# Kernel tuning notes

Hardware: AMD Instinct MI355X
Metric: run time of the kernel (lower is better)

Reference implementation:

```python
import jax, jax.numpy as jnp
import numpy as np

N_HEAD = 16
ROPE_BASE = 10000.0


def _rotate_half(x):
    # interleaved rotate: (-x2, x1) pairs, matching torch stack+flatten
    x1 = x[..., ::2]
    x2 = x[..., 1::2]
    return jnp.stack((-x2, x1), axis=-1).reshape(x.shape)


def setup_inputs() -> dict:
    key = jax.random.key(0)
    ks = jax.random.split(key, 5)
    B, S, C = 4, 2048, 1024
    sc = 1.0 / np.sqrt(C)
    return {
        "x": jax.random.normal(ks[0], (B, S, C), jnp.float32),
        "W_qkv": jax.random.normal(ks[1], (C, 3 * C), jnp.float32) * sc,
        "b_qkv": jax.random.normal(ks[2], (3 * C,), jnp.float32) * 0.02,
        "W_proj": jax.random.normal(ks[3], (C, C), jnp.float32) * sc,
        "b_proj": jax.random.normal(ks[4], (C,), jnp.float32) * 0.02,
    }


def reference(x, W_qkv, b_qkv, W_proj, b_proj):
    B, S, C = x.shape
    H = N_HEAD
    D = C // H

    qkv = x @ W_qkv + b_qkv                       # [B,S,3C]
    q, k, v = jnp.split(qkv, 3, axis=-1)
    q = q.reshape(B, S, H, D).transpose(0, 2, 1, 3)  # [B,H,S,D]
    k = k.reshape(B, S, H, D).transpose(0, 2, 1, 3)
    v = v.reshape(B, S, H, D).transpose(0, 2, 1, 3)

    # RoPE cache (offset=0), faithful to source: emb = cat(freqs, freqs)
    inv_freq = 1.0 / (ROPE_BASE ** (jnp.arange(0, D, 2, dtype=jnp.float32) / D))
    pos = jnp.arange(S, dtype=jnp.float32)
    freqs = jnp.outer(pos, inv_freq)              # [S, D/2]
    emb = jnp.concatenate((freqs, freqs), axis=-1)  # [S, D]
    cos = jnp.cos(emb)[None, None, :, :]
    sin = jnp.sin(emb)[None, None, :, :]

    q = q * cos + _rotate_half(q) * sin
    k = k * cos + _rotate_half(k) * sin

    scale = 1.0 / jnp.sqrt(jnp.asarray(D, x.dtype))
    scores = jnp.einsum("bhqd,bhkd->bhqk", q, k) * scale  # [B,H,S,S]
    causal = jnp.tril(jnp.ones((S, S), dtype=bool))
    scores = jnp.where(causal[None, None], scores, jnp.asarray(-jnp.inf, x.dtype))
    att = jax.nn.softmax(scores, axis=-1)
    out = jnp.einsum("bhqk,bhkd->bhqd", att, v)    # [B,H,S,D]

    out = out.transpose(0, 2, 1, 3).reshape(B, S, C)
    out = out @ W_proj + b_proj                    # dropout=0 (eval)
    return out
```

## Files before the change

kernel.cpp:

```cpp
#include <hip/hip_runtime.h>
#include <hip/hip_bf16.h>
#include <math.h>

#define B_ 4
#define S_ 2048
#define C_ 1024
#define H_ 16
#define D_ 64
#define M_ (B_*S_)
#define NQKV (3*C_)
#define KDIM C_

typedef float f32x4 __attribute__((ext_vector_type(4)));
typedef short bf16x8 __attribute__((ext_vector_type(8)));

static __device__ __forceinline__ ushort f2bf(float f){
    __hip_bfloat16 h = __float2bfloat16(f);
    union { __hip_bfloat16 b; ushort u; } v; v.b = h;
    return v.u;
}

static __device__ __forceinline__ void gload16(const ushort* g, ushort* l){
    __builtin_amdgcn_global_load_lds((__attribute__((address_space(1))) void*)g,
                                     (__attribute__((address_space(3))) void*)l,
                                     16, 0, 0);
}

__global__ void k_conv(const float* __restrict__ in, ushort* __restrict__ out, int n4){
    int i = blockIdx.x*blockDim.x + threadIdx.x;
    if (i < n4){
        float4 v = *(const float4*)(in + i*4);
        ushort4 o;
        o.x = f2bf(v.x); o.y = f2bf(v.y); o.z = f2bf(v.z); o.w = f2bf(v.w);
        *(ushort4*)(out + i*4) = o;
    }
}

__global__ void k_transpose(const float* __restrict__ in, ushort* __restrict__ out,
                            int R, int Ccol){
    __shared__ float tile[32][33];
    int c0 = blockIdx.x*32, r0 = blockIdx.y*32;
    int tx = threadIdx.x, ty = threadIdx.y;
    for (int j = ty; j < 32; j += 8)
        tile[j][tx] = in[(r0 + j)*Ccol + c0 + tx];
    __syncthreads();
    for (int j = ty; j < 32; j += 8)
        out[(size_t)(c0 + tx)*R + r0 + j] = f2bf(tile[j][tx]);
}

__global__ void k_rope_tab(float* __restrict__ cosT, float* __restrict__ sinT){
    int t = blockIdx.x*blockDim.x + threadIdx.x;
    if (t >= S_*D_) return;
    int pos = t >> 6, j = t & 63;
    float invf = powf(10000.0f, -(float)(j & 31) / 32.0f);
    float ang = (float)pos * invf;
    cosT[t] = cosf(ang);
    sinT[t] = sinf(ang);
}


__launch_bounds__(512, 4)
__global__ void k_qkv(const ushort* __restrict__ xb, const ushort* __restrict__ wt,
                      const float* __restrict__ bqkv,
                      const float* __restrict__ cosT, const float* __restrict__ sinT,
                      ushort* __restrict__ qb, ushort* __restrict__ kb, ushort* __restrict__ vT){
    __shared__ __align__(16) ushort As[2][256][32];
    __shared__ __align__(16) ushort Bs[2][128][32];
    int bid = blockIdx.x;
    int lin = (bid & 7)*96 + (bid >> 3);
    int bx = lin % 24, by = lin / 24;
    int M0 = by*256, N0 = bx*128;
    int tid = threadIdx.x;
    int wid = tid >> 6, lane = tid & 63;
    int wm = wid >> 1, wn = wid & 1;
    int lrow = lane & 15, lk = lane >> 4;
    int swu = (lrow >> 1) & 3;

    int scol = (((lane & 3) ^ ((lane >> 3) & 3))) * 8;
    const ushort* gA0 = &xb[(size_t)(M0 + wid*16 + (lane >> 2))*KDIM + scol];
    const ushort* gA1 = gA0 + (size_t)128*KDIM;
    const ushort* gB0 = &wt[(size_t)(N0 + wid*16 + (lane >> 2))*KDIM + scol];

    f32x4 acc[4][4] = {};
    int cur = 0;
    gload16(gA0, &As[0][wid*16][0]);
    gload16(gA1, &As[0][128 + wid*16][0]);
    gload16(gB0, &Bs[0][wid*16][0]);
    __syncthreads();

    for (int k0 = 0; k0 < KDIM; k0 += 32){
        int nk = k0 + 32;
        if (nk < KDIM){
            gload16(gA0 + nk, &As[cur^1][wid*16][0]);
            gload16(gA1 + nk, &As[cur^1][128 + wid*16][0]);
            gload16(gB0 + nk, &Bs[cur^1][wid*16][0]);
        }
        bf16x8 a[4], b[4];
#pragma unroll
        for (int mi = 0; mi < 4; mi++)
            a[mi] = *(const bf16x8*)(&As[cur][wm*64 + mi*16 + lrow][(lk ^ swu)*8]);
#pragma unroll
        for (int ni = 0; ni < 4; ni++)
            b[ni] = *(const bf16x8*)(&Bs[cur][wn*64 + ni*16 + lrow][(lk ^ swu)*8]);
#pragma unroll
        for (int mi = 0; mi < 4; mi++)
#pragma unroll
            for (int ni = 0; ni < 4; ni++)
                acc[mi][ni] = __builtin_amdgcn_mfma_f32_16x16x32_bf16(a[mi], b[ni], acc[mi][ni], 0, 0, 0);
        __syncthreads();
        cur ^= 1;
    }
#pragma unroll
    for (int mi = 0; mi < 4; mi++)
#pragma unroll
    for (int ni = 0; ni < 4; ni++){
        int gn = N0 + wn*64 + ni*16 + lrow;
        float bias = bqkv[gn];
        int which = gn >> 10;
        int cn = gn & 1023;
        int h = cn >> 6, d = cn & 63;
        int gm0 = M0 + wm*64 + mi*16 + lk*4;
        if (which == 2){
            int bb = gm0 >> 11, pos0 = gm0 & 2047;
            ushort4 o = { f2bf(acc[mi][ni][0] + bias), f2bf(acc[mi][ni][1] + bias),
                          f2bf(acc[mi][ni][2] + bias), f2bf(acc[mi][ni][3] + bias) };
            *(ushort4*)(&vT[(((size_t)(bb*H_ + h))*D_ + d)*S_ + pos0]) = o;
        } else {
#pragma unroll
            for (int rr = 0; rr < 4; rr++){
                int gm = gm0 + rr;
                float val = acc[mi][ni][rr] + bias;
                float rot = __shfl_xor(val, 1);
                int bb = gm >> 11, pos = gm & 2047;
                int out_idx = ((((bb*H_ + h)*S_) + pos))*D_ + d;
                float c = cosT[pos*64 + d], s = sinT[pos*64 + d];
                float o = val*c + ((d & 1) ? rot : -rot)*s;
                if (which == 0) o *= 0.18033688f;
                ((which == 0) ? qb : kb)[out_idx] = f2bf(o);
            }
        }
    }
}

__launch_bounds__(512, 4)
__global__ void k_proj(const ushort* __restrict__ ab, const ushort* __restrict__ wt,
                       const float* __restrict__ bias, float* __restrict__ out){
    __shared__ __align__(16) ushort As[2][256][32];
    __shared__ __align__(16) ushort Bs[2][128][32];
    int bid = blockIdx.x;
    int lin = (bid & 7)*32 + (bid >> 3);
    int bx = lin & 7, by = lin >> 3;
    int M0 = by*256, N0 = bx*128;
    int tid = threadIdx.x;
    int wid = tid >> 6, lane = tid & 63;
    int wm = wid >> 1, wn = wid & 1;
    int lrow = lane & 15, lk = lane >> 4;
    int swu = (lrow >> 1) & 3;

    int scol = (((lane & 3) ^ ((lane >> 3) & 3))) * 8;
    const ushort* gA0 = &ab[(size_t)(M0 + wid*16 + (lane >> 2))*KDIM + scol];
    const ushort* gA1 = gA0 + (size_t)128*KDIM;
    const ushort* gB0 = &wt[(size_t)(N0 + wid*16 + (lane >> 2))*KDIM + scol];

    f32x4 acc[4][4] = {};
    int cur = 0;
    gload16(gA0, &As[0][wid*16][0]);
    gload16(gA1, &As[0][128 + wid*16][0]);
    gload16(gB0, &Bs[0][wid*16][0]);
    __syncthreads();

    for (int k0 = 0; k0 < KDIM; k0 += 32){
        int nk = k0 + 32;
        if (nk < KDIM){
            gload16(gA0 + nk, &As[cur^1][wid*16][0]);
            gload16(gA1 + nk, &As[cur^1][128 + wid*16][0]);
            gload16(gB0 + nk, &Bs[cur^1][wid*16][0]);
        }
        bf16x8 a[4], b[4];
#pragma unroll
        for (int mi = 0; mi < 4; mi++)
            a[mi] = *(const bf16x8*)(&As[cur][wm*64 + mi*16 + lrow][(lk ^ swu)*8]);
#pragma unroll
        for (int ni = 0; ni < 4; ni++)
            b[ni] = *(const bf16x8*)(&Bs[cur][wn*64 + ni*16 + lrow][(lk ^ swu)*8]);
#pragma unroll
        for (int mi = 0; mi < 4; mi++)
#pragma unroll
            for (int ni = 0; ni < 4; ni++)
                acc[mi][ni] = __builtin_amdgcn_mfma_f32_16x16x32_bf16(a[mi], b[ni], acc[mi][ni], 0, 0, 0);
        __syncthreads();
        cur ^= 1;
    }
#pragma unroll
    for (int mi = 0; mi < 4; mi++)
#pragma unroll
    for (int ni = 0; ni < 4; ni++){
        int gn = N0 + wn*64 + ni*16 + lrow;
        float bv = bias[gn];
#pragma unroll
        for (int rr = 0; rr < 4; rr++){
            int gm = M0 + wm*64 + mi*16 + lk*4 + rr;
            out[(size_t)gm*C_ + gn] = acc[mi][ni][rr] + bv;
        }
    }
}

__launch_bounds__(256)
__global__ void k_attn(const ushort* __restrict__ qb, const ushort* __restrict__ kb,
                       const ushort* __restrict__ vT, ushort* __restrict__ ob){
    __shared__ __align__(16) ushort Ks[64][64];
    __shared__ __align__(16) ushort Vs[64][64];
    __shared__ __align__(16) ushort ptile[4][16][64];
    int bh = blockIdx.x;
    int qt = (gridDim.y - 1) - blockIdx.y;
    int bb = bh >> 4, h = bh & 15;
    int tid = threadIdx.x, wid = tid >> 6, lane = tid & 63;
    int lrow = lane & 15, lk = lane >> 4;
    int sw = lrow & 7;
    const ushort* qp = qb + (size_t)bh*S_*D_;
    const ushort* kp = kb + (size_t)bh*S_*D_;
    const ushort* vp = vT + (size_t)bh*D_*S_;
    int qrow = qt*64 + wid*16 + lrow;

    bf16x8 fq[2];
    fq[0] = *(const bf16x8*)(&qp[qrow*D_ + lk*8]);
    fq[1] = *(const bf16x8*)(&qp[qrow*D_ + 32 + lk*8]);

    f32x4 acc[4] = {};
    float m = -1e30f, l = 0.0f;

    int tr  = tid >> 3;
    int tcu = tid & 7;
    int twu = (tcu ^ (tr & 7)) * 8;
    int tc  = tcu * 8;

    int4 ra = *(const int4*)(&kp[tr*D_ + tc]);
    int4 rb = *(const int4*)(&kp[(tr + 32)*D_ + tc]);
    int4 rc = *(const int4*)(&vp[(size_t)tr*S_ + tc]);
    int4 rd = *(const int4*)(&vp[(size_t)(tr + 32)*S_ + tc]);

    const int jend = qt*64;
    for (int j0 = 0; ; j0 += 64){
        *(int4*)(&Ks[tr][twu])      = ra;
        *(int4*)(&Ks[tr + 32][twu]) = rb;
        *(int4*)(&Vs[tr][twu])      = rc;
        *(int4*)(&Vs[tr + 32][twu]) = rd;
        __syncthreads();
        bool diag = (j0 == jend);
        if (!diag){
            int j1 = j0 + 64;
            ra = *(const int4*)(&kp[(j1 + tr)*D_ + tc]);
            rb = *(const int4*)(&kp[(j1 + tr + 32)*D_ + tc]);
            rc = *(const int4*)(&vp[(size_t)tr*S_ + j1 + tc]);
            rd = *(const int4*)(&vp[(size_t)(tr + 32)*S_ + j1 + tc]);
        }

        float p[4][4];
        float tmax = -1e30f;
        if (!diag){
#pragma unroll
            for (int s2 = 0; s2 < 4; s2++){
                bf16x8 k0 = *(const bf16x8*)(&Ks[s2*16 + lrow][(lk ^ sw)*8]);
                bf16x8 k1 = *(const bf16x8*)(&Ks[s2*16 + lrow][((4 + lk) ^ sw)*8]);
                f32x4 z = {};
                z = __builtin_amdgcn_mfma_f32_16x16x32_bf16(k0, fq[0], z, 0, 0, 0);
                z = __builtin_amdgcn_mfma_f32_16x16x32_bf16(k1, fq[1], z, 0, 0, 0);
#pragma unroll
                for (int r = 0; r < 4; r++){ p[s2][r] = z[r]; tmax = fmaxf(tmax, z[r]); }
            }
        } else {
#pragma unroll
            for (int s2 = 0; s2 < 4; s2++){
                if (s2 <= wid){
                    bf16x8 k0 = *(const bf16x8*)(&Ks[s2*16 + lrow][(lk ^ sw)*8]);
                    bf16x8 k1 = *(const bf16x8*)(&Ks[s2*16 + lrow][((4 + lk) ^ sw)*8]);
                    f32x4 z = {};
                    z = __builtin_amdgcn_mfma_f32_16x16x32_bf16(k0, fq[0], z, 0, 0, 0);
                    z = __builtin_amdgcn_mfma_f32_16x16x32_bf16(k1, fq[1], z, 0, 0, 0);
#pragma unroll
                    for (int r = 0; r < 4; r++){
                        float v = z[r];
                        if (s2 == wid && (lk*4 + r) > lrow) v = -1e30f;
                        p[s2][r] = v; tmax = fmaxf(tmax, v);
                    }
                } else {
#pragma unroll
                    for (int r = 0; r < 4; r++) p[s2][r] = -1e30f;
                }
            }
        }
        tmax = fmaxf(tmax, __shfl_xor(tmax, 16));
        tmax = fmaxf(tmax, __shfl_xor(tmax, 32));
        if (__any(tmax > m)){
            float newm = fmaxf(m, tmax);
            float resc = exp2f(m - newm);
            m = newm;
            l *= resc;
#pragma unroll
            for (int nt = 0; nt < 4; nt++)
#pragma unroll
                for (int r = 0; r < 4; r++) acc[nt][r] *= resc;
        }
        float rsum = 0.0f;
#pragma unroll
        for (int s2 = 0; s2 < 4; s2++)
#pragma unroll
            for (int r = 0; r < 4; r++){
                float e = exp2f(p[s2][r] - m);
                p[s2][r] = e;
                rsum += e;
            }
        rsum += __shfl_xor(rsum, 16);
        rsum += __shfl_xor(rsum, 32);
        l += rsum;

#pragma unroll
        for (int s2 = 0; s2 < 4; s2++){
            uint2 w;
            w.x = (unsigned)f2bf(p[s2][0]) | ((unsigned)f2bf(p[s2][1]) << 16);
            w.y = (unsigned)f2bf(p[s2][2]) | ((unsigned)f2bf(p[s2][3]) << 16);
            *(uint2*)(&ptile[wid][lrow][((s2*2 + (lk >> 1)) ^ sw)*8 + (lk & 1)*4]) = w;
        }
        bool hi = !diag || (wid >= 2);
        bf16x8 fp0 = *(const bf16x8*)(&ptile[wid][lrow][(lk ^ sw)*8]);
#pragma unroll
        for (int nt = 0; nt < 4; nt++){
            bf16x8 fv0 = *(const bf16x8*)(&Vs[nt*16 + lrow][(lk ^ sw)*8]);
            acc[nt] = __builtin_amdgcn_mfma_f32_16x16x32_bf16(fv0, fp0, acc[nt], 0, 0, 0);
        }
        if (hi){
            bf16x8 fp1 = *(const bf16x8*)(&ptile[wid][lrow][((4 + lk) ^ sw)*8]);
#pragma unroll
            for (int nt = 0; nt < 4; nt++){
                bf16x8 fv1 = *(const bf16x8*)(&Vs[nt*16 + lrow][((4 + lk) ^ sw)*8]);
                acc[nt] = __builtin_amdgcn_mfma_f32_16x16x32_bf16(fv1, fp1, acc[nt], 0, 0, 0);
            }
        }
        __syncthreads();
        if (diag) break;
    }
    float rl = 1.0f / l;
#pragma unroll
    for (int nt = 0; nt < 4; nt++){
        ushort4 o = { f2bf(acc[nt][0]*rl), f2bf(acc[nt][1]*rl),
                      f2bf(acc[nt][2]*rl), f2bf(acc[nt][3]*rl) };
        *(ushort4*)(&ob[((size_t)(bb*S_ + qrow))*C_ + h*D_ + nt*16 + lk*4]) = o;
    }
}

extern "C" void kernel_launch(void* const* d_in, const int* in_sizes, int n_in,
                              void* d_out, int out_size, void* d_ws, size_t ws_size,
                              hipStream_t stream) {
    const float* x     = (const float*)d_in[0];
    const float* Wqkv  = (const float*)d_in[1];
    const float* bqkv  = (const float*)d_in[2];
    const float* Wproj = (const float*)d_in[3];
    const float* bproj = (const float*)d_in[4];
    float* out = (float*)d_out;

    char* ws = (char*)d_ws;
    ushort* xb   = (ushort*)(ws);
    ushort* wqt  = (ushort*)(ws + (16u<<20));
    ushort* wpt  = (ushort*)(ws + (22u<<20));
    float*  cosT = (float*) (ws + (24u<<20));
    float*  sinT = (float*) (ws + (24u<<20) + (512u<<10));
    ushort* qbuf = (ushort*)(ws + (25u<<20));
    ushort* kbuf = (ushort*)(ws + (41u<<20));
    ushort* vbuf = (ushort*)(ws + (57u<<20));
    ushort* obuf = (ushort*)(ws + (73u<<20));

    k_conv<<<(M_*KDIM/4 + 255)/256, 256, 0, stream>>>(x, xb, M_*KDIM/4);
    dim3 tb(32, 8);
    k_transpose<<<dim3(NQKV/32, KDIM/32), tb, 0, stream>>>(Wqkv, wqt, KDIM, NQKV);
    k_transpose<<<dim3(C_/32, KDIM/32), tb, 0, stream>>>(Wproj, wpt, KDIM, C_);
    k_rope_tab<<<(S_*D_ + 255)/256, 256, 0, stream>>>(cosT, sinT);

    k_qkv<<<768, 512, 0, stream>>>(xb, wqt, bqkv, cosT, sinT, qbuf, kbuf, vbuf);
    k_attn<<<dim3(B_*H_, S_/64), 256, 0, stream>>>(qbuf, kbuf, vbuf, obuf);
    k_proj<<<256, 512, 0, stream>>>(obuf, wpt, bproj, out);
}
```

Baseline: 201.3 us.

## Rewrite attention with 32x32 MFMA, 128-row query tiles, register-resident P

The attention kernel now processes 128 query rows per block, with each wave owning 32 rows, and uses 32x32x16 bf16 MFMAs instead of 16x16x32. The softmax probabilities are packed with v_cvt_pk_bf16_f32 and rearranged across lanes with permlane32_swap, so they feed the PV MFMA directly and the LDS P tile round-trip is gone. Each K/V tile loaded into shared memory is now reused by twice as many query rows, cutting global and LDS traffic per query. The costs are higher register pressure, a 3-blocks-per-SM launch bound, half as many blocks (worse load balance on the causal triangle), and waves idling on key tiles past their diagonal.

```diff
diff --git a/kernel.cpp b/kernel.cpp
--- a/kernel.cpp
+++ b/kernel.cpp
@@ -12,6 +12,7 @@
 #define KDIM C_
 
 typedef float f32x4 __attribute__((ext_vector_type(4)));
+typedef float f32x16 __attribute__((ext_vector_type(16)));
 typedef short bf16x8 __attribute__((ext_vector_type(8)));
 
 static __device__ __forceinline__ ushort f2bf(float f){
@@ -57,7 +58,6 @@
     cosT[t] = cosf(ang);
     sinT[t] = sinf(ang);
 }
-
 
 __launch_bounds__(512, 4)
 __global__ void k_qkv(const ushort* __restrict__ xb, const ushort* __restrict__ wt,
@@ -205,146 +205,143 @@
     }
 }
 
-__launch_bounds__(256)
+__launch_bounds__(256, 3)
 __global__ void k_attn(const ushort* __restrict__ qb, const ushort* __restrict__ kb,
                        const ushort* __restrict__ vT, ushort* __restrict__ ob){
     __shared__ __align__(16) ushort Ks[64][64];
     __shared__ __align__(16) ushort Vs[64][64];
-    __shared__ __align__(16) ushort ptile[4][16][64];
     int bh = blockIdx.x;
     int qt = (gridDim.y - 1) - blockIdx.y;
     int bb = bh >> 4, h = bh & 15;
     int tid = threadIdx.x, wid = tid >> 6, lane = tid & 63;
-    int lrow = lane & 15, lk = lane >> 4;
-    int sw = lrow & 7;
+    int lq = lane & 31, hi = lane >> 5;
     const ushort* qp = qb + (size_t)bh*S_*D_;
     const ushort* kp = kb + (size_t)bh*S_*D_;
     const ushort* vp = vT + (size_t)bh*D_*S_;
-    int qrow = qt*64 + wid*16 + lrow;
-
-    bf16x8 fq[2];
-    fq[0] = *(const bf16x8*)(&qp[qrow*D_ + lk*8]);
-    fq[1] = *(const bf16x8*)(&qp[qrow*D_ + 32 + lk*8]);
-
-    f32x4 acc[4] = {};
+    int qw = qt*128 + wid*32;
+    int qrow = qw + lq;
+    int swz = lq & 7;
+
+    bf16x8 fq[4];
+#pragma unroll
+    for (int c = 0; c < 4; c++)
+        fq[c] = *(const bf16x8*)(&qp[qrow*D_ + c*16 + hi*8]);
+
+    f32x16 acc0 = {}, acc1 = {};
     float m = -1e30f, l = 0.0f;
 
-    int tr  = tid >> 3;
-    int tcu = tid & 7;
+    int tr = tid >> 3, tcu = tid & 7;
     int twu = (tcu ^ (tr & 7)) * 8;
-    int tc  = tcu * 8;
+    int tc = tcu * 8;
 
     int4 ra = *(const int4*)(&kp[tr*D_ + tc]);
-    int4 rb = *(const int4*)(&kp[(tr + 32)*D_ + tc]);
+    int4 rb = *(const int4*)(&kp[(tr+32)*D_ + tc]);
     int4 rc = *(const int4*)(&vp[(size_t)tr*S_ + tc]);
-    int4 rd = *(const int4*)(&vp[(size_t)(tr + 32)*S_ + tc]);
-
-    const int jend = qt*64;
-    for (int j0 = 0; ; j0 += 64){
-        *(int4*)(&Ks[tr][twu])      = ra;
-        *(int4*)(&Ks[tr + 32][twu]) = rb;
-        *(int4*)(&Vs[tr][twu])      = rc;
-        *(int4*)(&Vs[tr + 32][twu]) = rd;
+    int4 rd = *(const int4*)(&vp[(size_t)(tr+32)*S_ + tc]);
+
+    int nit = 2*qt + 2;
+    for (int it = 0; it < nit; ++it){
+        int j0 = it*64;
+        *(int4*)(&Ks[tr][twu])    = ra;
+        *(int4*)(&Ks[tr+32][twu]) = rb;
+        *(int4*)(&Vs[tr][twu])    = rc;
+        *(int4*)(&Vs[tr+32][twu]) = rd;
         __syncthreads();
-        bool diag = (j0 == jend);
-        if (!diag){
+        if (it + 1 < nit){
             int j1 = j0 + 64;
-            ra = *(const int4*)(&kp[(j1 + tr)*D_ + tc]);
-            rb = *(const int4*)(&kp[(j1 + tr + 32)*D_ + tc]);
+            ra = *(const int4*)(&kp[(j1+tr)*D_ + tc]);
+            rb = *(const int4*)(&kp[(j1+tr+32)*D_ + tc]);
             rc = *(const int4*)(&vp[(size_t)tr*S_ + j1 + tc]);
-            rd = *(const int4*)(&vp[(size_t)(tr + 32)*S_ + j1 + tc]);
-        }
-
-        float p[4][4];
-        float tmax = -1e30f;
-        if (!diag){
-#pragma unroll
-            for (int s2 = 0; s2 < 4; s2++){
-                bf16x8 k0 = *(const bf16x8*)(&Ks[s2*16 + lrow][(lk ^ sw)*8]);
-                bf16x8 k1 = *(const bf16x8*)(&Ks[s2*16 + lrow][((4 + lk) ^ sw)*8]);
-                f32x4 z = {};
-                z = __builtin_amdgcn_mfma_f32_16x16x32_bf16(k0, fq[0], z, 0, 0, 0);
-                z = __builtin_amdgcn_mfma_f32_16x16x32_bf16(k1, fq[1], z, 0, 0, 0);
-#pragma unroll
-                for (int r = 0; r < 4; r++){ p[s2][r] = z[r]; tmax = fmaxf(tmax, z[r]); }
-            }
-        } else {
-#pragma unroll
-            for (int s2 = 0; s2 < 4; s2++){
-                if (s2 <= wid){
-                    bf16x8 k0 = *(const bf16x8*)(&Ks[s2*16 + lrow][(lk ^ sw)*8]);
-                    bf16x8 k1 = *(const bf16x8*)(&Ks[s2*16 + lrow][((4 + lk) ^ sw)*8]);
-                    f32x4 z = {};
-                    z = __builtin_amdgcn_mfma_f32_16x16x32_bf16(k0, fq[0], z, 0, 0, 0);
-                    z = __builtin_amdgcn_mfma_f32_16x16x32_bf16(k1, fq[1], z, 0, 0, 0);
-#pragma unroll
-                    for (int r = 0; r < 4; r++){
-                        float v = z[r];
-                        if (s2 == wid && (lk*4 + r) > lrow) v = -1e30f;
-                        p[s2][r] = v; tmax = fmaxf(tmax, v);
-                    }
-                } else {
-#pragma unroll
-                    for (int r = 0; r < 4; r++) p[s2][r] = -1e30f;
+            rd = *(const int4*)(&vp[(size_t)(tr+32)*S_ + j1 + tc]);
+        }
+        int rel = qw - j0;
+        if (rel >= 0){
+            bool diag0 = (rel == 0);
+            bool have1 = (rel >= 32);
+            bool diag1 = (rel == 32);
+            f32x16 z0 = {}, z1 = {};
+#pragma unroll
+            for (int c = 0; c < 4; c++){
+                bf16x8 kf = *(const bf16x8*)(&Ks[lq][((2*c + hi) ^ swz)*8]);
+                z0 = __builtin_amdgcn_mfma_f32_32x32x16_bf16(kf, fq[c], z0, 0, 0, 0);
+            }
+            if (have1){
+#pragma unroll
+                for (int c = 0; c < 4; c++){
+                    bf16x8 kf = *(const bf16x8*)(&Ks[32 + lq][((2*c + hi) ^ swz)*8]);
+                    z1 = __builtin_amdgcn_mfma_f32_32x32x16_bf16(kf, fq[c], z1, 0, 0, 0);
                 }
             }
-        }
-        tmax = fmaxf(tmax, __shfl_xor(tmax, 16));
-        tmax = fmaxf(tmax, __shfl_xor(tmax, 32));
-        if (__any(tmax > m)){
-            float newm = fmaxf(m, tmax);
-            float resc = exp2f(m - newm);
-            m = newm;
-            l *= resc;
-#pragma unroll
-            for (int nt = 0; nt < 4; nt++)
-#pragma unroll
-                for (int r = 0; r < 4; r++) acc[nt][r] *= resc;
-        }
-        float rsum = 0.0f;
-#pragma unroll
-        for (int s2 = 0; s2 < 4; s2++)
-#pragma unroll
-            for (int r = 0; r < 4; r++){
-                float e = exp2f(p[s2][r] - m);
-                p[s2][r] = e;
-                rsum += e;
-            }
-        rsum += __shfl_xor(rsum, 16);
-        rsum += __shfl_xor(rsum, 32);
-        l += rsum;
-
-#pragma unroll
-        for (int s2 = 0; s2 < 4; s2++){
-            uint2 w;
-            w.x = (unsigned)f2bf(p[s2][0]) | ((unsigned)f2bf(p[s2][1]) << 16);
-            w.y = (unsigned)f2bf(p[s2][2]) | ((unsigned)f2bf(p[s2][3]) << 16);
-            *(uint2*)(&ptile[wid][lrow][((s2*2 + (lk >> 1)) ^ sw)*8 + (lk & 1)*4]) = w;
-        }
-        bool hi = !diag || (wid >= 2);
-        bf16x8 fp0 = *(const bf16x8*)(&ptile[wid][lrow][(lk ^ sw)*8]);
-#pragma unroll
-        for (int nt = 0; nt < 4; nt++){
-            bf16x8 fv0 = *(const bf16x8*)(&Vs[nt*16 + lrow][(lk ^ sw)*8]);
-            acc[nt] = __builtin_amdgcn_mfma_f32_16x16x32_bf16(fv0, fp0, acc[nt], 0, 0, 0);
-        }
-        if (hi){
-            bf16x8 fp1 = *(const bf16x8*)(&ptile[wid][lrow][((4 + lk) ^ sw)*8]);
-#pragma unroll
-            for (int nt = 0; nt < 4; nt++){
-                bf16x8 fv1 = *(const bf16x8*)(&Vs[nt*16 + lrow][((4 + lk) ^ sw)*8]);
-                acc[nt] = __builtin_amdgcn_mfma_f32_16x16x32_bf16(fv1, fp1, acc[nt], 0, 0, 0);
-            }
+            if (diag0){
+#pragma unroll
+                for (int r = 0; r < 16; r++)
+                    if (((r & 3) + 8*(r >> 2) + 4*hi) > lq) z0[r] = -1e30f;
+            }
+            if (diag1){
+#pragma unroll
+                for (int r = 0; r < 16; r++)
+                    if (((r & 3) + 8*(r >> 2) + 4*hi) > lq) z1[r] = -1e30f;
+            }
+            float tmax = z0[0];
+#pragma unroll
+            for (int r = 1; r < 16; r++) tmax = fmaxf(tmax, z0[r]);
+            if (have1){
+#pragma unroll
+                for (int r = 0; r < 16; r++) tmax = fmaxf(tmax, z1[r]);
+            }
+            tmax = fmaxf(tmax, __shfl_xor(tmax, 32));
+            if (__any(tmax > m)){
+                float newm = fmaxf(m, tmax);
+                float resc = exp2f(m - newm);
+                m = newm; l *= resc;
+#pragma unroll
+                for (int r = 0; r < 16; r++){ acc0[r] *= resc; acc1[r] *= resc; }
+            }
+            float rsum = 0.0f;
+#pragma unroll
+            for (int r = 0; r < 16; r++){ z0[r] = exp2f(z0[r] - m); rsum += z0[r]; }
+            if (have1){
+#pragma unroll
+                for (int r = 0; r < 16; r++){ z1[r] = exp2f(z1[r] - m); rsum += z1[r]; }
+            }
+            rsum += __shfl_xor(rsum, 32);
+            l += rsum;
+
+#define PV_SUB(zz, r0_, su, t) do {                                              \
+    unsigned w0, w1, w2, w3;                                                     \
+    asm("v_cvt_pk_bf16_f32 %0, %1, %2" : "=v"(w0) : "v"(zz[r0_+0]), "v"(zz[r0_+1])); \
+    asm("v_cvt_pk_bf16_f32 %0, %1, %2" : "=v"(w1) : "v"(zz[r0_+2]), "v"(zz[r0_+3])); \
+    asm("v_cvt_pk_bf16_f32 %0, %1, %2" : "=v"(w2) : "v"(zz[r0_+4]), "v"(zz[r0_+5])); \
+    asm("v_cvt_pk_bf16_f32 %0, %1, %2" : "=v"(w3) : "v"(zz[r0_+6]), "v"(zz[r0_+7])); \
+    auto s02 = __builtin_amdgcn_permlane32_swap(w0, w2, false, false);            \
+    auto s13 = __builtin_amdgcn_permlane32_swap(w1, w3, false, false);            \
+    union { unsigned u[4]; bf16x8 v; } pf;                                       \
+    pf.u[0] = s02[0]; pf.u[1] = s13[0]; pf.u[2] = s02[1]; pf.u[3] = s13[1];      \
+    bf16x8 vf0 = *(const bf16x8*)(&Vs[lq][(((su)*4 + (t)*2 + hi) ^ swz)*8]);     \
+    acc0 = __builtin_amdgcn_mfma_f32_32x32x16_bf16(vf0, pf.v, acc0, 0, 0, 0);    \
+    bf16x8 vf1 = *(const bf16x8*)(&Vs[32 + lq][(((su)*4 + (t)*2 + hi) ^ swz)*8]);\
+    acc1 = __builtin_amdgcn_mfma_f32_32x32x16_bf16(vf1, pf.v, acc1, 0, 0, 0);    \
+} while(0)
+
+            PV_SUB(z0, 0, 0, 0);
+            PV_SUB(z0, 8, 0, 1);
+            if (have1){
+                PV_SUB(z1, 0, 1, 0);
+                PV_SUB(z1, 8, 1, 1);
+            }
+#undef PV_SUB
         }
         __syncthreads();
-        if (diag) break;
     }
     float rl = 1.0f / l;
 #pragma unroll
-    for (int nt = 0; nt < 4; nt++){
-        ushort4 o = { f2bf(acc[nt][0]*rl), f2bf(acc[nt][1]*rl),
-                      f2bf(acc[nt][2]*rl), f2bf(acc[nt][3]*rl) };
-        *(ushort4*)(&ob[((size_t)(bb*S_ + qrow))*C_ + h*D_ + nt*16 + lk*4]) = o;
+    for (int rg = 0; rg < 4; rg++){
+        ushort4 o0 = { f2bf(acc0[rg*4+0]*rl), f2bf(acc0[rg*4+1]*rl),
+                       f2bf(acc0[rg*4+2]*rl), f2bf(acc0[rg*4+3]*rl) };
+        *(ushort4*)(&ob[((size_t)(bb*S_ + qrow))*C_ + h*D_ + rg*8 + hi*4]) = o0;
+        ushort4 o1 = { f2bf(acc1[rg*4+0]*rl), f2bf(acc1[rg*4+1]*rl),
+                       f2bf(acc1[rg*4+2]*rl), f2bf(acc1[rg*4+3]*rl) };
+        *(ushort4*)(&ob[((size_t)(bb*S_ + qrow))*C_ + h*D_ + 32 + rg*8 + hi*4]) = o1;
     }
 }
 
@@ -376,6 +373,6 @@
     k_rope_tab<<<(S_*D_ + 255)/256, 256, 0, stream>>>(cosT, sinT);
 
     k_qkv<<<768, 512, 0, stream>>>(xb, wqt, bqkv, cosT, sinT, qbuf, kbuf, vbuf);
-    k_attn<<<dim3(B_*H_, S_/64), 256, 0, stream>>>(qbuf, kbuf, vbuf, obuf);
+    k_attn<<<dim3(B_*H_, S_/128), 256, 0, stream>>>(qbuf, kbuf, vbuf, obuf);
     k_proj<<<256, 512, 0, stream>>>(obuf, wpt, bproj, out);
 }
```

New measurement: 190.4 us. -5.4%, faster.
